# Optimization experiments

Hardware: AMD Instinct MI355X
Metric: run time of the kernel (lower is better)

The kernel has to match this reference:

```python
import jax, jax.numpy as jnp
import numpy as np

DIM_Q = 256
DIM_K = 256
DIM_V = 256
NUM_HEADS = 4


def setup_inputs() -> dict:
    key = jax.random.key(0)
    ks = jax.random.split(key, 12)
    B, NQ, NK = 4, 2048, 2048
    s_in = 1.0 / np.sqrt(DIM_Q)
    s_v = 1.0 / np.sqrt(DIM_V)
    return {
        "Q": jax.random.normal(ks[0], (B, NQ, DIM_Q), jnp.float32),
        "K": jax.random.normal(ks[1], (B, NK, DIM_K), jnp.float32),
        "Wq": jax.random.normal(ks[2], (DIM_V, DIM_Q), jnp.float32) * s_in,
        "bq": jnp.zeros((DIM_V,), jnp.float32),
        "Wk": jax.random.normal(ks[3], (DIM_V, DIM_K), jnp.float32) * s_in,
        "bk": jnp.zeros((DIM_V,), jnp.float32),
        "Wv": jax.random.normal(ks[4], (DIM_V, DIM_K), jnp.float32) * s_in,
        "bv": jnp.zeros((DIM_V,), jnp.float32),
        "Wo": jax.random.normal(ks[5], (DIM_V, DIM_V), jnp.float32) * s_v,
        "bo": jnp.zeros((DIM_V,), jnp.float32),
        "g0": jnp.ones((DIM_V,), jnp.float32),
        "b0": jnp.zeros((DIM_V,), jnp.float32),
        "g1": jnp.ones((DIM_V,), jnp.float32),
        "b1": jnp.zeros((DIM_V,), jnp.float32),
    }


def _layernorm(x, g, b, eps=1e-5):
    mu = jnp.mean(x, axis=-1, keepdims=True)
    var = jnp.mean(jnp.square(x - mu), axis=-1, keepdims=True)
    return (x - mu) * jax.lax.rsqrt(var + eps) * g + b


def _mab(Q, K, Wq, bq, Wk, bk, Wv, bv, Wo, bo, g0, b0, g1, b1):
    B, NQ, _ = Q.shape
    H = NUM_HEADS
    Dh = DIM_V // H  # head dim
    q = jnp.einsum("bqd,ed->bqe", Q, Wq) + bq  # (B,NQ,DV)
    k = jnp.einsum("bkd,ed->bke", K, Wk) + bk
    v = jnp.einsum("bkd,ed->bke", K, Wv) + bv
    # split heads: (B,S,H,Dh) -> (B,H,S,Dh)
    qh = q.reshape(B, NQ, H, Dh).transpose(0, 2, 1, 3)
    kh = k.reshape(B, -1, H, Dh).transpose(0, 2, 1, 3)
    vh = v.reshape(B, -1, H, Dh).transpose(0, 2, 1, 3)
    # NOTE: original scales by sqrt(dim_V), not sqrt(head_dim)
    scores = jnp.einsum("bhqd,bhkd->bhqk", qh, kh) / np.sqrt(DIM_V)
    A = jax.nn.softmax(scores, axis=-1)
    oh = qh + jnp.einsum("bhqk,bhkd->bhqd", A, vh)  # residual with projected Q
    O = oh.transpose(0, 2, 1, 3).reshape(B, NQ, DIM_V)
    O = _layernorm(O, g0, b0)
    O = O + jax.nn.relu(jnp.einsum("bqd,ed->bqe", O, Wo) + bo)
    O = _layernorm(O, g1, b1)
    return O


def reference(Q, K, Wq, bq, Wk, bk, Wv, bv, Wo, bo, g0, b0, g1, b1):
    return _mab(Q, K, Wq, bq, Wk, bk, Wv, bv, Wo, bo, g0, b0, g1, b1)
```

## Files before the change

### kernel.cpp

```cpp
#include <hip/hip_runtime.h>
#include <hip/hip_bf16.h>
#include <math.h>


typedef __attribute__((ext_vector_type(8))) short bf16x8;
typedef __attribute__((ext_vector_type(4))) float f32x4;

static __device__ __forceinline__ unsigned short f2bf(float x) {
  return __bfloat16_as_ushort(__float2bfloat16(x));
}
static __device__ __forceinline__ int pk2(float lo, float hi) {
  return (int)((unsigned)f2bf(lo) | ((unsigned)f2bf(hi) << 16));
}
static __device__ __forceinline__ float exp2_fast(float x) {
  float r; asm("v_exp_f32 %0, %1" : "=v"(r) : "v"(x)); return r;
}

#define SWZ(row, col) ((col) ^ (((row) & 7) << 3))

__global__ __launch_bounds__(256, 2) void proj_kernel(
    const float* __restrict__ Q, const float* __restrict__ K,
    const float* __restrict__ Wq, const float* __restrict__ bq,
    const float* __restrict__ Wk, const float* __restrict__ bk,
    const float* __restrict__ Wv, const float* __restrict__ bv,
    float* __restrict__ qout, unsigned short* __restrict__ kbf,
    unsigned short* __restrict__ vtb)
{
  __shared__ __align__(16) unsigned short Ab[64][64];
  __shared__ __align__(16) unsigned short Wb[64][64];
  const int tid = threadIdx.x;
  const int z = blockIdx.z;
  const int bn = blockIdx.x, bm = blockIdx.y;

  const float* A    = (z == 0) ? Q  : K;
  const float* W    = (z == 0) ? Wq : ((z == 1) ? Wk : Wv);
  const float* bias = (z == 0) ? bq : ((z == 1) ? bk : bv);

  const int wid = tid >> 6, lane = tid & 63;
  const int l15 = lane & 15, g = lane >> 4;
  const int wr = wid >> 1, wc = wid & 1;
  const float* Ablk = A + (size_t)bm * 64 * 256;
  const float* Wblk = W + (size_t)bn * 64 * 256;

  const int sr = tid >> 2, sc = (tid & 3) * 16;
  const int c0 = SWZ(sr, sc), c1 = SWZ(sr, sc + 8);

  f32x4 acc[2][2];
  #pragma unroll
  for (int i = 0; i < 2; ++i)
    #pragma unroll
    for (int j = 0; j < 2; ++j)
      #pragma unroll
      for (int r = 0; r < 4; ++r) acc[i][j][r] = 0.f;

  float4 aR[4], wR[4];
  #pragma unroll
  for (int u = 0; u < 4; ++u) {
    aR[u] = *(const float4*)(Ablk + (size_t)sr*256 + sc + u*4);
    wR[u] = *(const float4*)(Wblk + (size_t)sr*256 + sc + u*4);
  }

  for (int k0 = 0; k0 < 256; k0 += 64) {
    if (k0) __syncthreads();
    int4 pa0 = { pk2(aR[0].x,aR[0].y), pk2(aR[0].z,aR[0].w),
                 pk2(aR[1].x,aR[1].y), pk2(aR[1].z,aR[1].w) };
    int4 pa1 = { pk2(aR[2].x,aR[2].y), pk2(aR[2].z,aR[2].w),
                 pk2(aR[3].x,aR[3].y), pk2(aR[3].z,aR[3].w) };
    int4 pw0 = { pk2(wR[0].x,wR[0].y), pk2(wR[0].z,wR[0].w),
                 pk2(wR[1].x,wR[1].y), pk2(wR[1].z,wR[1].w) };
    int4 pw1 = { pk2(wR[2].x,wR[2].y), pk2(wR[2].z,wR[2].w),
                 pk2(wR[3].x,wR[3].y), pk2(wR[3].z,wR[3].w) };
    *(int4*)&Ab[sr][c0] = pa0;  *(int4*)&Ab[sr][c1] = pa1;
    *(int4*)&Wb[sr][c0] = pw0;  *(int4*)&Wb[sr][c1] = pw1;
    __syncthreads();
    if (k0 < 192) {
      #pragma unroll
      for (int u = 0; u < 4; ++u) {
        aR[u] = *(const float4*)(Ablk + (size_t)sr*256 + (k0+64) + sc + u*4);
        wR[u] = *(const float4*)(Wblk + (size_t)sr*256 + (k0+64) + sc + u*4);
      }
    }
    const unsigned short (*Ta)[64] = (z == 2) ? Wb : Ab;
    const unsigned short (*Tb)[64] = (z == 2) ? Ab : Wb;
    __builtin_amdgcn_s_setprio(1);
    #pragma unroll
    for (int kc = 0; kc < 64; kc += 32) {
      bf16x8 af[2], bf_[2];
      #pragma unroll
      for (int i = 0; i < 2; ++i) {
        int ra = wr*32 + i*16 + l15;
        int rb = wc*32 + i*16 + l15;
        af[i]  = *(const bf16x8*)&Ta[ra][SWZ(ra, kc + g*8)];
        bf_[i] = *(const bf16x8*)&Tb[rb][SWZ(rb, kc + g*8)];
      }
      #pragma unroll
      for (int i = 0; i < 2; ++i)
        #pragma unroll
        for (int j = 0; j < 2; ++j)
          acc[i][j] = __builtin_amdgcn_mfma_f32_16x16x32_bf16(af[i], bf_[j], acc[i][j], 0, 0, 0);
    }
    __builtin_amdgcn_s_setprio(0);
  }

  if (z == 2) {
    const int bvb = bm >> 5;
    const int n0 = (bm & 31) * 64 + wc*32;
    #pragma unroll
    for (int di = 0; di < 2; ++di)
      #pragma unroll
      for (int r = 0; r < 4; ++r) {
        int d = wr*32 + di*16 + g*4 + r;
        float bvs = bias[bn*64 + d];
        #pragma unroll
        for (int ni = 0; ni < 2; ++ni) {
          float c = acc[di][ni][r] + bvs;
          vtb[((size_t)(bvb*4 + bn)*64 + d)*2048 + n0 + ni*16 + l15] = f2bf(c);
        }
      }
    return;
  }

  const int gm = bm*64 + wr*32, ge = bn*64 + wc*32;
  float bv0 = bias[ge + l15], bv1 = bias[ge + 16 + l15];
  #pragma unroll
  for (int mi = 0; mi < 2; ++mi)
    #pragma unroll
    for (int r = 0; r < 4; ++r) {
      int row = gm + mi*16 + g*4 + r;
      #pragma unroll
      for (int ei = 0; ei < 2; ++ei) {
        float c = acc[mi][ei][r] + (ei ? bv1 : bv0);
        if (z == 0) qout[(size_t)row*256 + ge + ei*16 + l15] = c;
        else        kbf [(size_t)row*256 + ge + ei*16 + l15] = f2bf(c);
      }
    }
}

typedef unsigned short tile64_t[64][64];

__global__ __launch_bounds__(512, 4) void attn_mfma6(
    const float* __restrict__ q,
    const unsigned short* __restrict__ kb,
    const unsigned short* __restrict__ vt,
    float* __restrict__ o)
{
  extern __shared__ __align__(16) char smem_dyn[];
  tile64_t* Ks = (tile64_t*)smem_dyn;
  tile64_t* Vt = (tile64_t*)(smem_dyn + 32768);

  const int tid = threadIdx.x;
  const int wid = tid >> 6;
  const int grp = wid >> 2;
  const int w4  = wid & 3;
  const int lane = tid & 63;
  const int l15 = lane & 15;
  const int g = lane >> 4;
  const int lin = blockIdx.x;
  const int xcd = lin & 7, idx = lin >> 3;
  const int bh = xcd * 2 + (idx >> 5);
  const int qb = idx & 31;
  const int b = bh >> 2, h = bh & 3;

  const float qscale = 0.0625f * 1.44269504089f;
  bf16x8 qf[2];
  {
    const float* qp = q + ((size_t)(b*2048 + qb*64 + w4*16 + l15))*256 + h*64;
    #pragma unroll
    for (int ds_ = 0; ds_ < 2; ++ds_) {
      union { bf16x8 v; unsigned short s[8]; } tmp;
      #pragma unroll
      for (int j = 0; j < 8; ++j) tmp.s[j] = f2bf(qp[ds_*32 + g*8 + j] * qscale);
      qf[ds_] = tmp.v;
    }
  }

  const int gt = tid & 255;
  const int sr = gt >> 2, sc = (gt & 3) * 16;
  const int c0 = SWZ(sr, sc), c1 = SWZ(sr, sc + 8);
  const unsigned short* kgp = kb + ((size_t)(b*2048 + grp*1024 + sr))*256 + h*64 + sc;
  const unsigned short* vgp = vt + ((size_t)bh*64 + sr)*2048 + grp*1024 + sc;

  f32x4 oa[4];
  #pragma unroll
  for (int mt = 0; mt < 4; ++mt)
    #pragma unroll
    for (int r = 0; r < 4; ++r) oa[mt][r] = 0.f;
  float l_ = 0.f;

  {
    int4 k0_ = *(const int4*)kgp, k1_ = *(const int4*)(kgp + 8);
    int4 v0_ = *(const int4*)vgp, v1_ = *(const int4*)(vgp + 8);
    *(int4*)&Ks[grp*2+0][sr][c0] = k0_;  *(int4*)&Ks[grp*2+0][sr][c1] = k1_;
    *(int4*)&Vt[grp*2+0][sr][c0] = v0_;  *(int4*)&Vt[grp*2+0][sr][c1] = v1_;
  }
  int4 kA0 = *(const int4*)(kgp + (size_t)64*256);
  int4 kA1 = *(const int4*)(kgp + (size_t)64*256 + 8);
  int4 vA0 = *(const int4*)(vgp + 64);
  int4 vA1 = *(const int4*)(vgp + 64 + 8);
  __syncthreads();

  for (int kt = 0; kt < 16; ++kt) {
    const int cur = kt & 1;
    const tile64_t& Kc = Ks[grp*2 + cur];
    const tile64_t& Vc = Vt[grp*2 + cur];

    f32x4 sa[4];
    #pragma unroll
    for (int mt = 0; mt < 4; ++mt)
      #pragma unroll
      for (int r = 0; r < 4; ++r) sa[mt][r] = 0.f;
    __builtin_amdgcn_s_setprio(1);
    #pragma unroll
    for (int ds_ = 0; ds_ < 2; ++ds_) {
      #pragma unroll
      for (int mt = 0; mt < 4; ++mt) {
        bf16x8 af = *(const bf16x8*)&Kc[mt*16 + l15][SWZ(l15, ds_*32 + g*8)];
        sa[mt] = __builtin_amdgcn_mfma_f32_16x16x32_bf16(af, qf[ds_], sa[mt], 0, 0, 0);
      }
    }
    __builtin_amdgcn_s_setprio(0);

    float ps = 0.f;
    unsigned pk01[4], pk23[4];
    #pragma unroll
    for (int mt = 0; mt < 4; ++mt) {
      float p0 = exp2_fast(sa[mt][0]);
      float p1 = exp2_fast(sa[mt][1]);
      float p2 = exp2_fast(sa[mt][2]);
      float p3 = exp2_fast(sa[mt][3]);
      ps += (p0 + p1) + (p2 + p3);
      pk01[mt] = (unsigned)pk2(p0, p1);
      pk23[mt] = (unsigned)pk2(p2, p3);
    }
    ps += __shfl_xor(ps, 16, 64);
    ps += __shfl_xor(ps, 32, 64);
    l_ += ps;

    __builtin_amdgcn_s_setprio(1);
    #pragma unroll
    for (int ks_ = 0; ks_ < 2; ++ks_) {
      unsigned a0 = pk01[2*ks_], b0 = pk01[2*ks_ + 1];
      unsigned a1 = pk23[2*ks_], b1 = pk23[2*ks_ + 1];
      asm volatile("v_permlane32_swap_b32 %0, %1" : "+v"(a0), "+v"(b0));
      asm volatile("v_permlane16_swap_b32 %0, %1" : "+v"(a0), "+v"(b0));
      asm volatile("v_permlane32_swap_b32 %0, %1" : "+v"(a1), "+v"(b1));
      asm volatile("v_permlane16_swap_b32 %0, %1" : "+v"(a1), "+v"(b1));
      int4 pw = { (int)a0, (int)a1, (int)b0, (int)b1 };
      bf16x8 pf = __builtin_bit_cast(bf16x8, pw);
      #pragma unroll
      for (int mt = 0; mt < 4; ++mt) {
        bf16x8 vf = *(const bf16x8*)&Vc[mt*16 + l15][SWZ(l15, ks_*32 + g*8)];
        oa[mt] = __builtin_amdgcn_mfma_f32_16x16x32_bf16(vf, pf, oa[mt], 0, 0, 0);
      }
    }
    __builtin_amdgcn_s_setprio(0);

    if (kt < 15) {
      *(int4*)&Ks[grp*2+(cur^1)][sr][c0] = kA0;
      *(int4*)&Ks[grp*2+(cur^1)][sr][c1] = kA1;
      *(int4*)&Vt[grp*2+(cur^1)][sr][c0] = vA0;
      *(int4*)&Vt[grp*2+(cur^1)][sr][c1] = vA1;
      if (kt < 14) {
        const unsigned short* kn = kgp + (size_t)(kt + 2) * 64 * 256;
        const unsigned short* vn = vgp + (kt + 2) * 64;
        kA0 = *(const int4*)kn;  kA1 = *(const int4*)(kn + 8);
        vA0 = *(const int4*)vn;  vA1 = *(const int4*)(vn + 8);
      }
    }
    __syncthreads();
  }

  float* cob = (float*)smem_dyn;
  float* cml = (float*)(smem_dyn + 32768);
  const int ci = w4*64 + lane;
  if (grp == 1) {
    #pragma unroll
    for (int mt = 0; mt < 4; ++mt)
      #pragma unroll
      for (int r = 0; r < 4; ++r) cob[(mt*4 + r)*256 + ci] = oa[mt][r];
    cml[ci] = l_;
  }
  __syncthreads();
  if (grp == 0) {
    float linv = 1.0f / (l_ + cml[ci]);
    float* op = o + ((size_t)(b*2048 + qb*64 + w4*16 + l15))*256 + h*64;
    #pragma unroll
    for (int mt = 0; mt < 4; ++mt) {
      int dbase = mt*16 + g*4;
      float4 qv = *(const float4*)(op + dbase);
      float4 st;
      st.x = qv.x + (oa[mt][0] + cob[(mt*4+0)*256 + ci]) * linv;
      st.y = qv.y + (oa[mt][1] + cob[(mt*4+1)*256 + ci]) * linv;
      st.z = qv.z + (oa[mt][2] + cob[(mt*4+2)*256 + ci]) * linv;
      st.w = qv.w + (oa[mt][3] + cob[(mt*4+3)*256 + ci]) * linv;
      *(float4*)(op + dbase) = st;
    }
  }
}

__global__ __launch_bounds__(512) void fused_out(
    const float* __restrict__ x, const float* __restrict__ Wo,
    const float* __restrict__ bo,
    const float* __restrict__ g0v, const float* __restrict__ b0v,
    const float* __restrict__ g1v, const float* __restrict__ b1v,
    float* __restrict__ y)
{
  __shared__ __align__(16) unsigned short As[32][256];
  __shared__ __align__(16) unsigned short Ws[256][64];
  __shared__ float mu_[32], rs_[32];
  float* P = (float*)&Ws[0][0];

  const int tid = threadIdx.x;
  const int w = tid >> 6, lane = tid & 63;
  const int l15 = lane & 15, g = lane >> 4;
  const int r0 = blockIdx.x * 32;

  {
    float4 g4 = *(const float4*)(g0v + lane*4);
    float4 b4 = *(const float4*)(b0v + lane*4);
    #pragma unroll
    for (int rr = 0; rr < 4; ++rr) {
      int m = w*4 + rr;
      const float* xr = x + (size_t)(r0 + m) * 256;
      float4 v = *(const float4*)(xr + lane*4);
      float s = v.x + v.y + v.z + v.w;
      #pragma unroll
      for (int mk = 1; mk <= 32; mk <<= 1) s += __shfl_xor(s, mk, 64);
      float mu = s * (1.0f/256.0f);
      float dx = v.x-mu, dy = v.y-mu, dz = v.z-mu, dw = v.w-mu;
      float qq = dx*dx + dy*dy + dz*dz + dw*dw;
      #pragma unroll
      for (int mk = 1; mk <= 32; mk <<= 1) qq += __shfl_xor(qq, mk, 64);
      float rstd = rsqrtf(qq * (1.0f/256.0f) + 1e-5f);
      if (lane == 0) { mu_[m] = mu; rs_[m] = rstd; }
      float nx = dx*rstd*g4.x + b4.x;
      float ny = dy*rstd*g4.y + b4.y;
      float nz = dz*rstd*g4.z + b4.z;
      float nw = dw*rstd*g4.w + b4.w;
      int2 pv = { pk2(nx, ny), pk2(nz, nw) };
      int col = lane*4;
      *(int2*)&As[m][SWZ(m, col)] = pv;
    }
  }
  __syncthreads();

  const int m0 = (w >> 2) * 16;
  const int e0 = (w & 3) * 64;
  f32x4 acc4[4];
  #pragma unroll
  for (int j = 0; j < 4; ++j)
    #pragma unroll
    for (int r = 0; r < 4; ++r) acc4[j][r] = 0.f;

  for (int k0 = 0; k0 < 256; k0 += 64) {
    if (k0) __syncthreads();
    {
      const int ch = tid & 7;
      const int er = tid >> 3;
      #pragma unroll
      for (int p = 0; p < 4; ++p) {
        int e = p*64 + er;
        const float* wp = Wo + (size_t)e*256 + k0 + ch*8;
        float4 u0 = *(const float4*)wp;
        float4 u1 = *(const float4*)(wp + 4);
        int4 pk = { pk2(u0.x,u0.y), pk2(u0.z,u0.w), pk2(u1.x,u1.y), pk2(u1.z,u1.w) };
        *(int4*)&Ws[e][SWZ(e, ch*8)] = pk;
      }
    }
    __syncthreads();
    __builtin_amdgcn_s_setprio(1);
    #pragma unroll
    for (int ds_ = 0; ds_ < 2; ++ds_) {
      int ma = m0 + l15;
      bf16x8 af = *(const bf16x8*)&As[ma][SWZ(ma, k0 + ds_*32 + g*8)];
      #pragma unroll
      for (int j = 0; j < 4; ++j) {
        int er = e0 + j*16 + l15;
        bf16x8 bfv = *(const bf16x8*)&Ws[er][SWZ(er, ds_*32 + g*8)];
        acc4[j] = __builtin_amdgcn_mfma_f32_16x16x32_bf16(af, bfv, acc4[j], 0, 0, 0);
      }
    }
    __builtin_amdgcn_s_setprio(0);
  }
  __syncthreads();

  #pragma unroll
  for (int j = 0; j < 4; ++j) {
    int e = e0 + j*16 + l15;
    float bov = bo[e], g0e = g0v[e], b0e = b0v[e];
    #pragma unroll
    for (int r = 0; r < 4; ++r) {
      int m = m0 + g*4 + r;
      float xv = x[(size_t)(r0 + m)*256 + e];
      float resv = (xv - mu_[m]) * rs_[m] * g0e + b0e;
      float val = acc4[j][r] + bov;
      P[m*256 + e] = resv + fmaxf(val, 0.f);
    }
  }
  __syncthreads();

  {
    float4 g4 = *(const float4*)(g1v + lane*4);
    float4 b4 = *(const float4*)(b1v + lane*4);
    #pragma unroll
    for (int rr = 0; rr < 4; ++rr) {
      int m = w*4 + rr;
      float4 v = *(const float4*)&P[m*256 + lane*4];
      float s = v.x + v.y + v.z + v.w;
      #pragma unroll
      for (int mk = 1; mk <= 32; mk <<= 1) s += __shfl_xor(s, mk, 64);
      float mu = s * (1.0f/256.0f);
      float dx = v.x-mu, dy = v.y-mu, dz = v.z-mu, dw = v.w-mu;
      float qq = dx*dx + dy*dy + dz*dz + dw*dw;
      #pragma unroll
      for (int mk = 1; mk <= 32; mk <<= 1) qq += __shfl_xor(qq, mk, 64);
      float rstd = rsqrtf(qq * (1.0f/256.0f) + 1e-5f);
      float4 o;
      o.x = dx*rstd*g4.x + b4.x; o.y = dy*rstd*g4.y + b4.y;
      o.z = dz*rstd*g4.z + b4.z; o.w = dw*rstd*g4.w + b4.w;
      *(float4*)(y + (size_t)(r0 + m)*256 + lane*4) = o;
    }
  }
}

extern "C" void kernel_launch(void* const* d_in, const int* in_sizes, int n_in,
                              void* d_out, int out_size, void* d_ws, size_t ws_size,
                              hipStream_t stream) {
  const float* Q  = (const float*)d_in[0];
  const float* K  = (const float*)d_in[1];
  const float* Wq = (const float*)d_in[2];
  const float* bq = (const float*)d_in[3];
  const float* Wk = (const float*)d_in[4];
  const float* bk = (const float*)d_in[5];
  const float* Wv = (const float*)d_in[6];
  const float* bv = (const float*)d_in[7];
  const float* Wo = (const float*)d_in[8];
  const float* bo = (const float*)d_in[9];
  const float* g0 = (const float*)d_in[10];
  const float* b0 = (const float*)d_in[11];
  const float* g1 = (const float*)d_in[12];
  const float* b1 = (const float*)d_in[13];
  float* out = (float*)d_out;

  const size_t SZ = (size_t)4 * 2048 * 256;
  if (ws_size < 2 * SZ * sizeof(unsigned short)) return;

  unsigned short* kbf = (unsigned short*)d_ws;
  unsigned short* vtb = kbf + SZ;

  const int ATTN_LDS = 65536;
  hipFuncSetAttribute((const void*)attn_mfma6,
                      hipFuncAttributeMaxDynamicSharedMemorySize, ATTN_LDS);

  proj_kernel<<<dim3(4, 128, 3), dim3(256), 0, stream>>>(
      Q, K, Wq, bq, Wk, bk, Wv, bv, out, kbf, vtb);
  attn_mfma6<<<dim3(512), dim3(512), ATTN_LDS, stream>>>(out, kbf, vtb, out);
  fused_out<<<dim3(256), dim3(512), 0, stream>>>(out, Wo, bo, g0, b0, g1, b1, out);
}
```

Baseline: 69.56 us.

## Split attention keys four ways with two query tiles per wave

The attention kernel now divides the 2048 keys among four wave-pair groups of 512 keys each, down from two groups of 1024. Each wave handles two 16-row query tiles, so every K/V fragment read from LDS feeds two MFMAs. The double-buffered LDS ring becomes a single buffer per group, refilled from register prefetch with a barrier at the start of each step. The partial sums from the three extra groups are combined through a padded LDS buffer. This is meant to improve LDS operand reuse and raise the MFMA-to-load ratio, at the cost of more accumulator registers, one extra barrier per iteration, and a larger cross-group reduction.

```diff
diff --git a/kernel.cpp b/kernel.cpp
--- a/kernel.cpp
+++ b/kernel.cpp
@@ -136,22 +136,22 @@
     }
 }
 
-typedef unsigned short tile64_t[64][64];
-
-__global__ __launch_bounds__(512, 4) void attn_mfma6(
+typedef unsigned short tileKV_t[64][64];
+
+__global__ __launch_bounds__(512, 4) void attn_mfma7(
     const float* __restrict__ q,
     const unsigned short* __restrict__ kb,
     const unsigned short* __restrict__ vt,
     float* __restrict__ o)
 {
   extern __shared__ __align__(16) char smem_dyn[];
-  tile64_t* Ks = (tile64_t*)smem_dyn;
-  tile64_t* Vt = (tile64_t*)(smem_dyn + 32768);
+  tileKV_t* Ks = (tileKV_t*)smem_dyn;
+  tileKV_t* Vt = (tileKV_t*)(smem_dyn + 32768);
 
   const int tid = threadIdx.x;
   const int wid = tid >> 6;
-  const int grp = wid >> 2;
-  const int w4  = wid & 3;
+  const int grp = wid >> 1;
+  const int qw  = wid & 1;
   const int lane = tid & 63;
   const int l15 = lane & 15;
   const int g = lane >> 4;
@@ -162,138 +162,166 @@
   const int b = bh >> 2, h = bh & 3;
 
   const float qscale = 0.0625f * 1.44269504089f;
-  bf16x8 qf[2];
-  {
-    const float* qp = q + ((size_t)(b*2048 + qb*64 + w4*16 + l15))*256 + h*64;
+  bf16x8 qf[2][2];
+  #pragma unroll
+  for (int qt = 0; qt < 2; ++qt) {
+    const float* qp = q + ((size_t)(b*2048 + qb*64 + qw*32 + qt*16 + l15))*256 + h*64;
     #pragma unroll
     for (int ds_ = 0; ds_ < 2; ++ds_) {
       union { bf16x8 v; unsigned short s[8]; } tmp;
       #pragma unroll
       for (int j = 0; j < 8; ++j) tmp.s[j] = f2bf(qp[ds_*32 + g*8 + j] * qscale);
-      qf[ds_] = tmp.v;
-    }
-  }
-
-  const int gt = tid & 255;
-  const int sr = gt >> 2, sc = (gt & 3) * 16;
-  const int c0 = SWZ(sr, sc), c1 = SWZ(sr, sc + 8);
-  const unsigned short* kgp = kb + ((size_t)(b*2048 + grp*1024 + sr))*256 + h*64 + sc;
-  const unsigned short* vgp = vt + ((size_t)bh*64 + sr)*2048 + grp*1024 + sc;
-
-  f32x4 oa[4];
-  #pragma unroll
-  for (int mt = 0; mt < 4; ++mt)
-    #pragma unroll
-    for (int r = 0; r < 4; ++r) oa[mt][r] = 0.f;
-  float l_ = 0.f;
-
-  {
-    int4 k0_ = *(const int4*)kgp, k1_ = *(const int4*)(kgp + 8);
-    int4 v0_ = *(const int4*)vgp, v1_ = *(const int4*)(vgp + 8);
-    *(int4*)&Ks[grp*2+0][sr][c0] = k0_;  *(int4*)&Ks[grp*2+0][sr][c1] = k1_;
-    *(int4*)&Vt[grp*2+0][sr][c0] = v0_;  *(int4*)&Vt[grp*2+0][sr][c1] = v1_;
-  }
-  int4 kA0 = *(const int4*)(kgp + (size_t)64*256);
-  int4 kA1 = *(const int4*)(kgp + (size_t)64*256 + 8);
-  int4 vA0 = *(const int4*)(vgp + 64);
-  int4 vA1 = *(const int4*)(vgp + 64 + 8);
+      qf[qt][ds_] = tmp.v;
+    }
+  }
+
+  const int gt = tid & 127;
+  const int srow = gt >> 1;
+  const int chs  = (gt & 1) * 32;
+  int wcol[4];
+  #pragma unroll
+  for (int j = 0; j < 4; ++j) wcol[j] = SWZ(srow, chs + 8*j);
+  const unsigned short* kgp = kb + ((size_t)(b*2048 + grp*512 + srow))*256 + h*64 + chs;
+  const unsigned short* vgp = vt + ((size_t)bh*64 + srow)*2048 + grp*512 + chs;
+
+  f32x4 oa[2][4];
+  #pragma unroll
+  for (int qt = 0; qt < 2; ++qt)
+    #pragma unroll
+    for (int mt = 0; mt < 4; ++mt)
+      #pragma unroll
+      for (int r = 0; r < 4; ++r) oa[qt][mt][r] = 0.f;
+  float l0 = 0.f, l1 = 0.f;
+
+  int4 kR[4], vR[4];
+  #pragma unroll
+  for (int j = 0; j < 4; ++j) {
+    kR[j] = *(const int4*)(kgp + 8*j);
+    vR[j] = *(const int4*)(vgp + 8*j);
+  }
+
+  for (int t = 0; t < 8; ++t) {
+    if (t) __syncthreads();
+    #pragma unroll
+    for (int j = 0; j < 4; ++j) *(int4*)&Ks[grp][srow][wcol[j]] = kR[j];
+    #pragma unroll
+    for (int j = 0; j < 4; ++j) *(int4*)&Vt[grp][srow][wcol[j]] = vR[j];
+    __syncthreads();
+    if (t < 7) {
+      #pragma unroll
+      for (int j = 0; j < 4; ++j)
+        kR[j] = *(const int4*)(kgp + (size_t)(t+1)*64*256 + 8*j);
+    }
+
+    f32x4 sa[2][4];
+    #pragma unroll
+    for (int qt = 0; qt < 2; ++qt)
+      #pragma unroll
+      for (int mt = 0; mt < 4; ++mt)
+        #pragma unroll
+        for (int r = 0; r < 4; ++r) sa[qt][mt][r] = 0.f;
+    __builtin_amdgcn_s_setprio(1);
+    #pragma unroll
+    for (int ds_ = 0; ds_ < 2; ++ds_) {
+      #pragma unroll
+      for (int mt = 0; mt < 4; ++mt) {
+        bf16x8 af = *(const bf16x8*)&Ks[grp][mt*16 + l15][SWZ(l15, ds_*32 + g*8)];
+        sa[0][mt] = __builtin_amdgcn_mfma_f32_16x16x32_bf16(af, qf[0][ds_], sa[0][mt], 0, 0, 0);
+        sa[1][mt] = __builtin_amdgcn_mfma_f32_16x16x32_bf16(af, qf[1][ds_], sa[1][mt], 0, 0, 0);
+      }
+    }
+    __builtin_amdgcn_s_setprio(0);
+
+    unsigned pk01[2][4], pk23[2][4];
+    #pragma unroll
+    for (int qt = 0; qt < 2; ++qt) {
+      float ps = 0.f;
+      #pragma unroll
+      for (int mt = 0; mt < 4; ++mt) {
+        float p0 = exp2_fast(sa[qt][mt][0]);
+        float p1 = exp2_fast(sa[qt][mt][1]);
+        float p2 = exp2_fast(sa[qt][mt][2]);
+        float p3 = exp2_fast(sa[qt][mt][3]);
+        ps += (p0 + p1) + (p2 + p3);
+        pk01[qt][mt] = (unsigned)pk2(p0, p1);
+        pk23[qt][mt] = (unsigned)pk2(p2, p3);
+      }
+      ps += __shfl_xor(ps, 16, 64);
+      ps += __shfl_xor(ps, 32, 64);
+      if (qt == 0) l0 += ps; else l1 += ps;
+    }
+
+    if (t < 7) {
+      #pragma unroll
+      for (int j = 0; j < 4; ++j)
+        vR[j] = *(const int4*)(vgp + (t+1)*64 + 8*j);
+    }
+
+    __builtin_amdgcn_s_setprio(1);
+    #pragma unroll
+    for (int ks_ = 0; ks_ < 2; ++ks_) {
+      bf16x8 pf[2];
+      #pragma unroll
+      for (int qt = 0; qt < 2; ++qt) {
+        unsigned a0 = pk01[qt][2*ks_], b0 = pk01[qt][2*ks_ + 1];
+        unsigned a1 = pk23[qt][2*ks_], b1 = pk23[qt][2*ks_ + 1];
+        asm volatile("v_permlane32_swap_b32 %0, %1" : "+v"(a0), "+v"(b0));
+        asm volatile("v_permlane16_swap_b32 %0, %1" : "+v"(a0), "+v"(b0));
+        asm volatile("v_permlane32_swap_b32 %0, %1" : "+v"(a1), "+v"(b1));
+        asm volatile("v_permlane16_swap_b32 %0, %1" : "+v"(a1), "+v"(b1));
+        int4 pw = { (int)a0, (int)a1, (int)b0, (int)b1 };
+        pf[qt] = __builtin_bit_cast(bf16x8, pw);
+      }
+      #pragma unroll
+      for (int mt = 0; mt < 4; ++mt) {
+        bf16x8 vf = *(const bf16x8*)&Vt[grp][mt*16 + l15][SWZ(l15, ks_*32 + g*8)];
+        oa[0][mt] = __builtin_amdgcn_mfma_f32_16x16x32_bf16(vf, pf[0], oa[0][mt], 0, 0, 0);
+        oa[1][mt] = __builtin_amdgcn_mfma_f32_16x16x32_bf16(vf, pf[1], oa[1][mt], 0, 0, 0);
+      }
+    }
+    __builtin_amdgcn_s_setprio(0);
+  }
+
   __syncthreads();
-
-  for (int kt = 0; kt < 16; ++kt) {
-    const int cur = kt & 1;
-    const tile64_t& Kc = Ks[grp*2 + cur];
-    const tile64_t& Vc = Vt[grp*2 + cur];
-
-    f32x4 sa[4];
-    #pragma unroll
-    for (int mt = 0; mt < 4; ++mt)
-      #pragma unroll
-      for (int r = 0; r < 4; ++r) sa[mt][r] = 0.f;
-    __builtin_amdgcn_s_setprio(1);
-    #pragma unroll
-    for (int ds_ = 0; ds_ < 2; ++ds_) {
-      #pragma unroll
-      for (int mt = 0; mt < 4; ++mt) {
-        bf16x8 af = *(const bf16x8*)&Kc[mt*16 + l15][SWZ(l15, ds_*32 + g*8)];
-        sa[mt] = __builtin_amdgcn_mfma_f32_16x16x32_bf16(af, qf[ds_], sa[mt], 0, 0, 0);
-      }
-    }
-    __builtin_amdgcn_s_setprio(0);
-
-    float ps = 0.f;
-    unsigned pk01[4], pk23[4];
-    #pragma unroll
-    for (int mt = 0; mt < 4; ++mt) {
-      float p0 = exp2_fast(sa[mt][0]);
-      float p1 = exp2_fast(sa[mt][1]);
-      float p2 = exp2_fast(sa[mt][2]);
-      float p3 = exp2_fast(sa[mt][3]);
-      ps += (p0 + p1) + (p2 + p3);
-      pk01[mt] = (unsigned)pk2(p0, p1);
-      pk23[mt] = (unsigned)pk2(p2, p3);
-    }
-    ps += __shfl_xor(ps, 16, 64);
-    ps += __shfl_xor(ps, 32, 64);
-    l_ += ps;
-
-    __builtin_amdgcn_s_setprio(1);
-    #pragma unroll
-    for (int ks_ = 0; ks_ < 2; ++ks_) {
-      unsigned a0 = pk01[2*ks_], b0 = pk01[2*ks_ + 1];
-      unsigned a1 = pk23[2*ks_], b1 = pk23[2*ks_ + 1];
-      asm volatile("v_permlane32_swap_b32 %0, %1" : "+v"(a0), "+v"(b0));
-      asm volatile("v_permlane16_swap_b32 %0, %1" : "+v"(a0), "+v"(b0));
-      asm volatile("v_permlane32_swap_b32 %0, %1" : "+v"(a1), "+v"(b1));
-      asm volatile("v_permlane16_swap_b32 %0, %1" : "+v"(a1), "+v"(b1));
-      int4 pw = { (int)a0, (int)a1, (int)b0, (int)b1 };
-      bf16x8 pf = __builtin_bit_cast(bf16x8, pw);
-      #pragma unroll
-      for (int mt = 0; mt < 4; ++mt) {
-        bf16x8 vf = *(const bf16x8*)&Vc[mt*16 + l15][SWZ(l15, ks_*32 + g*8)];
-        oa[mt] = __builtin_amdgcn_mfma_f32_16x16x32_bf16(vf, pf, oa[mt], 0, 0, 0);
-      }
-    }
-    __builtin_amdgcn_s_setprio(0);
-
-    if (kt < 15) {
-      *(int4*)&Ks[grp*2+(cur^1)][sr][c0] = kA0;
-      *(int4*)&Ks[grp*2+(cur^1)][sr][c1] = kA1;
-      *(int4*)&Vt[grp*2+(cur^1)][sr][c0] = vA0;
-      *(int4*)&Vt[grp*2+(cur^1)][sr][c1] = vA1;
-      if (kt < 14) {
-        const unsigned short* kn = kgp + (size_t)(kt + 2) * 64 * 256;
-        const unsigned short* vn = vgp + (kt + 2) * 64;
-        kA0 = *(const int4*)kn;  kA1 = *(const int4*)(kn + 8);
-        vA0 = *(const int4*)vn;  vA1 = *(const int4*)(vn + 8);
-      }
-    }
-    __syncthreads();
-  }
-
   float* cob = (float*)smem_dyn;
-  float* cml = (float*)(smem_dyn + 32768);
-  const int ci = w4*64 + lane;
-  if (grp == 1) {
-    #pragma unroll
-    for (int mt = 0; mt < 4; ++mt)
-      #pragma unroll
-      for (int r = 0; r < 4; ++r) cob[(mt*4 + r)*256 + ci] = oa[mt][r];
-    cml[ci] = l_;
+  float* cml = (float*)(smem_dyn + 3*64*65*4);
+  if (grp > 0) {
+    const int gi = grp - 1;
+    #pragma unroll
+    for (int qt = 0; qt < 2; ++qt) {
+      int qloc = qw*32 + qt*16 + l15;
+      #pragma unroll
+      for (int mt = 0; mt < 4; ++mt)
+        #pragma unroll
+        for (int r = 0; r < 4; ++r)
+          cob[(gi*64 + mt*16 + g*4 + r)*65 + qloc] = oa[qt][mt][r];
+      cml[gi*64 + qloc] = (qt == 0) ? l0 : l1;
+    }
   }
   __syncthreads();
   if (grp == 0) {
-    float linv = 1.0f / (l_ + cml[ci]);
-    float* op = o + ((size_t)(b*2048 + qb*64 + w4*16 + l15))*256 + h*64;
-    #pragma unroll
-    for (int mt = 0; mt < 4; ++mt) {
-      int dbase = mt*16 + g*4;
-      float4 qv = *(const float4*)(op + dbase);
-      float4 st;
-      st.x = qv.x + (oa[mt][0] + cob[(mt*4+0)*256 + ci]) * linv;
-      st.y = qv.y + (oa[mt][1] + cob[(mt*4+1)*256 + ci]) * linv;
-      st.z = qv.z + (oa[mt][2] + cob[(mt*4+2)*256 + ci]) * linv;
-      st.w = qv.w + (oa[mt][3] + cob[(mt*4+3)*256 + ci]) * linv;
-      *(float4*)(op + dbase) = st;
+    #pragma unroll
+    for (int qt = 0; qt < 2; ++qt) {
+      int qloc = qw*32 + qt*16 + l15;
+      float lsum = (qt == 0 ? l0 : l1)
+                 + cml[qloc] + cml[64 + qloc] + cml[128 + qloc];
+      float linv = 1.0f / lsum;
+      float* op = o + ((size_t)(b*2048 + qb*64 + qloc))*256 + h*64;
+      #pragma unroll
+      for (int mt = 0; mt < 4; ++mt) {
+        int dbase = mt*16 + g*4;
+        float4 qv = *(const float4*)(op + dbase);
+        float4 st;
+        #pragma unroll
+        for (int r = 0; r < 4; ++r) {
+          float s = oa[qt][mt][r]
+                  + cob[(0*64 + dbase + r)*65 + qloc]
+                  + cob[(1*64 + dbase + r)*65 + qloc]
+                  + cob[(2*64 + dbase + r)*65 + qloc];
+          ((float*)&st)[r] = ((const float*)&qv)[r] + s * linv;
+        }
+        *(float4*)(op + dbase) = st;
+      }
     }
   }
 }
@@ -449,11 +477,11 @@
   unsigned short* vtb = kbf + SZ;
 
   const int ATTN_LDS = 65536;
-  hipFuncSetAttribute((const void*)attn_mfma6,
+  hipFuncSetAttribute((const void*)attn_mfma7,
                       hipFuncAttributeMaxDynamicSharedMemorySize, ATTN_LDS);
 
   proj_kernel<<<dim3(4, 128, 3), dim3(256), 0, stream>>>(
       Q, K, Wq, bq, Wk, bk, Wv, bv, out, kbf, vtb);
-  attn_mfma6<<<dim3(512), dim3(512), ATTN_LDS, stream>>>(out, kbf, vtb, out);
+  attn_mfma7<<<dim3(512), dim3(512), ATTN_LDS, stream>>>(out, kbf, vtb, out);
   fused_out<<<dim3(256), dim3(512), 0, stream>>>(out, Wo, bo, g0, b0, g1, b1, out);
 }
```

New measurement: 125.8 us. +80.9%, slower.

## Keep full-K input row block resident in LDS and reuse across two output tiles

Applied to the files above, without the earlier changes.

The projection kernel now converts and stores the whole 64x256 input row block to LDS once, then loops over two output column tiles per block, halving the grid in x. This cuts redundant global reads and bf16 conversion of Q/K rows, which were previously repeated for each of four column tiles. In exchange the software prefetch of the next K-chunk into registers is removed, so weight loads are no longer overlapped with MFMA. LDS use per block also rises, and there are fewer blocks.

```diff
diff --git a/kernel.cpp b/kernel.cpp
--- a/kernel.cpp
+++ b/kernel.cpp
@@ -18,7 +18,9 @@
 
 #define SWZ(row, col) ((col) ^ (((row) & 7) << 3))
 
-__global__ __launch_bounds__(256, 2) void proj_kernel(
+typedef unsigned short tile64_t[64][64];
+
+__global__ __launch_bounds__(256, 2) void proj2_kernel(
     const float* __restrict__ Q, const float* __restrict__ K,
     const float* __restrict__ Wq, const float* __restrict__ bq,
     const float* __restrict__ Wk, const float* __restrict__ bk,
@@ -26,11 +28,11 @@
     float* __restrict__ qout, unsigned short* __restrict__ kbf,
     unsigned short* __restrict__ vtb)
 {
-  __shared__ __align__(16) unsigned short Ab[64][64];
+  __shared__ __align__(16) unsigned short Ab[64][256];
   __shared__ __align__(16) unsigned short Wb[64][64];
   const int tid = threadIdx.x;
   const int z = blockIdx.z;
-  const int bn = blockIdx.x, bm = blockIdx.y;
+  const int bm = blockIdx.y;
 
   const float* A    = (z == 0) ? Q  : K;
   const float* W    = (z == 0) ? Wq : ((z == 1) ? Wk : Wv);
@@ -40,103 +42,104 @@
   const int l15 = lane & 15, g = lane >> 4;
   const int wr = wid >> 1, wc = wid & 1;
   const float* Ablk = A + (size_t)bm * 64 * 256;
-  const float* Wblk = W + (size_t)bn * 64 * 256;
 
   const int sr = tid >> 2, sc = (tid & 3) * 16;
   const int c0 = SWZ(sr, sc), c1 = SWZ(sr, sc + 8);
 
-  f32x4 acc[2][2];
   #pragma unroll
-  for (int i = 0; i < 2; ++i)
-    #pragma unroll
-    for (int j = 0; j < 2; ++j)
-      #pragma unroll
-      for (int r = 0; r < 4; ++r) acc[i][j][r] = 0.f;
-
-  float4 aR[4], wR[4];
-  #pragma unroll
-  for (int u = 0; u < 4; ++u) {
-    aR[u] = *(const float4*)(Ablk + (size_t)sr*256 + sc + u*4);
-    wR[u] = *(const float4*)(Wblk + (size_t)sr*256 + sc + u*4);
-  }
-
-  for (int k0 = 0; k0 < 256; k0 += 64) {
-    if (k0) __syncthreads();
-    int4 pa0 = { pk2(aR[0].x,aR[0].y), pk2(aR[0].z,aR[0].w),
-                 pk2(aR[1].x,aR[1].y), pk2(aR[1].z,aR[1].w) };
-    int4 pa1 = { pk2(aR[2].x,aR[2].y), pk2(aR[2].z,aR[2].w),
-                 pk2(aR[3].x,aR[3].y), pk2(aR[3].z,aR[3].w) };
-    int4 pw0 = { pk2(wR[0].x,wR[0].y), pk2(wR[0].z,wR[0].w),
-                 pk2(wR[1].x,wR[1].y), pk2(wR[1].z,wR[1].w) };
-    int4 pw1 = { pk2(wR[2].x,wR[2].y), pk2(wR[2].z,wR[2].w),
-                 pk2(wR[3].x,wR[3].y), pk2(wR[3].z,wR[3].w) };
-    *(int4*)&Ab[sr][c0] = pa0;  *(int4*)&Ab[sr][c1] = pa1;
-    *(int4*)&Wb[sr][c0] = pw0;  *(int4*)&Wb[sr][c1] = pw1;
-    __syncthreads();
-    if (k0 < 192) {
-      #pragma unroll
-      for (int u = 0; u < 4; ++u) {
-        aR[u] = *(const float4*)(Ablk + (size_t)sr*256 + (k0+64) + sc + u*4);
-        wR[u] = *(const float4*)(Wblk + (size_t)sr*256 + (k0+64) + sc + u*4);
-      }
-    }
-    const unsigned short (*Ta)[64] = (z == 2) ? Wb : Ab;
-    const unsigned short (*Tb)[64] = (z == 2) ? Ab : Wb;
-    __builtin_amdgcn_s_setprio(1);
-    #pragma unroll
-    for (int kc = 0; kc < 64; kc += 32) {
-      bf16x8 af[2], bf_[2];
-      #pragma unroll
-      for (int i = 0; i < 2; ++i) {
-        int ra = wr*32 + i*16 + l15;
-        int rb = wc*32 + i*16 + l15;
-        af[i]  = *(const bf16x8*)&Ta[ra][SWZ(ra, kc + g*8)];
-        bf_[i] = *(const bf16x8*)&Tb[rb][SWZ(rb, kc + g*8)];
-      }
-      #pragma unroll
-      for (int i = 0; i < 2; ++i)
+  for (int kb = 0; kb < 4; ++kb) {
+    const float* ap = Ablk + (size_t)sr*256 + kb*64 + sc;
+    float4 a0 = *(const float4*)ap,       a1 = *(const float4*)(ap + 4);
+    float4 a2 = *(const float4*)(ap + 8), a3 = *(const float4*)(ap + 12);
+    int4 p0 = { pk2(a0.x,a0.y), pk2(a0.z,a0.w), pk2(a1.x,a1.y), pk2(a1.z,a1.w) };
+    int4 p1 = { pk2(a2.x,a2.y), pk2(a2.z,a2.w), pk2(a3.x,a3.y), pk2(a3.z,a3.w) };
+    *(int4*)&Ab[sr][kb*64 + c0] = p0;
+    *(int4*)&Ab[sr][kb*64 + c1] = p1;
+  }
+
+  for (int bi = 0; bi < 2; ++bi) {
+    const int bn = blockIdx.x + bi*2;
+    const float* Wblk = W + (size_t)bn * 64 * 256;
+
+    f32x4 acc[2][2];
+    #pragma unroll
+    for (int i = 0; i < 2; ++i)
+      #pragma unroll
+      for (int j = 0; j < 2; ++j)
         #pragma unroll
-        for (int j = 0; j < 2; ++j)
-          acc[i][j] = __builtin_amdgcn_mfma_f32_16x16x32_bf16(af[i], bf_[j], acc[i][j], 0, 0, 0);
-    }
-    __builtin_amdgcn_s_setprio(0);
-  }
-
-  if (z == 2) {
-    const int bvb = bm >> 5;
-    const int n0 = (bm & 31) * 64 + wc*32;
-    #pragma unroll
-    for (int di = 0; di < 2; ++di)
-      #pragma unroll
-      for (int r = 0; r < 4; ++r) {
-        int d = wr*32 + di*16 + g*4 + r;
-        float bvs = bias[bn*64 + d];
+        for (int r = 0; r < 4; ++r) acc[i][j][r] = 0.f;
+
+    for (int k0 = 0; k0 < 256; k0 += 64) {
+      if (bi | k0) __syncthreads();
+      {
+        const float* wp = Wblk + (size_t)sr*256 + k0 + sc;
+        float4 w0 = *(const float4*)wp,       w1 = *(const float4*)(wp + 4);
+        float4 w2 = *(const float4*)(wp + 8), w3 = *(const float4*)(wp + 12);
+        int4 p0 = { pk2(w0.x,w0.y), pk2(w0.z,w0.w), pk2(w1.x,w1.y), pk2(w1.z,w1.w) };
+        int4 p1 = { pk2(w2.x,w2.y), pk2(w2.z,w2.w), pk2(w3.x,w3.y), pk2(w3.z,w3.w) };
+        *(int4*)&Wb[sr][c0] = p0;
+        *(int4*)&Wb[sr][c1] = p1;
+      }
+      __syncthreads();
+
+      __builtin_amdgcn_s_setprio(1);
+      #pragma unroll
+      for (int kc = 0; kc < 64; kc += 32) {
+        bf16x8 af[2], bf_[2];
         #pragma unroll
-        for (int ni = 0; ni < 2; ++ni) {
-          float c = acc[di][ni][r] + bvs;
-          vtb[((size_t)(bvb*4 + bn)*64 + d)*2048 + n0 + ni*16 + l15] = f2bf(c);
+        for (int i = 0; i < 2; ++i) {
+          int ra = wr*32 + i*16 + l15;
+          int rb = wc*32 + i*16 + l15;
+          if (z == 2) {
+            af[i]  = *(const bf16x8*)&Wb[ra][SWZ(ra, kc + g*8)];
+            bf_[i] = *(const bf16x8*)&Ab[rb][k0 + SWZ(rb, kc + g*8)];
+          } else {
+            af[i]  = *(const bf16x8*)&Ab[ra][k0 + SWZ(ra, kc + g*8)];
+            bf_[i] = *(const bf16x8*)&Wb[rb][SWZ(rb, kc + g*8)];
+          }
         }
-      }
-    return;
-  }
-
-  const int gm = bm*64 + wr*32, ge = bn*64 + wc*32;
-  float bv0 = bias[ge + l15], bv1 = bias[ge + 16 + l15];
-  #pragma unroll
-  for (int mi = 0; mi < 2; ++mi)
-    #pragma unroll
-    for (int r = 0; r < 4; ++r) {
-      int row = gm + mi*16 + g*4 + r;
-      #pragma unroll
-      for (int ei = 0; ei < 2; ++ei) {
-        float c = acc[mi][ei][r] + (ei ? bv1 : bv0);
-        if (z == 0) qout[(size_t)row*256 + ge + ei*16 + l15] = c;
-        else        kbf [(size_t)row*256 + ge + ei*16 + l15] = f2bf(c);
-      }
-    }
-}
-
-typedef unsigned short tile64_t[64][64];
+        #pragma unroll
+        for (int i = 0; i < 2; ++i)
+          #pragma unroll
+          for (int j = 0; j < 2; ++j)
+            acc[i][j] = __builtin_amdgcn_mfma_f32_16x16x32_bf16(af[i], bf_[j], acc[i][j], 0, 0, 0);
+      }
+      __builtin_amdgcn_s_setprio(0);
+    }
+
+    if (z == 2) {
+      const int bvb = bm >> 5;
+      const int n0 = (bm & 31) * 64 + wc*32;
+      #pragma unroll
+      for (int di = 0; di < 2; ++di)
+        #pragma unroll
+        for (int r = 0; r < 4; ++r) {
+          int d = wr*32 + di*16 + g*4 + r;
+          float bvs = bias[bn*64 + d];
+          #pragma unroll
+          for (int ni = 0; ni < 2; ++ni) {
+            float c = acc[di][ni][r] + bvs;
+            vtb[((size_t)(bvb*4 + bn)*64 + d)*2048 + n0 + ni*16 + l15] = f2bf(c);
+          }
+        }
+    } else {
+      const int gm = bm*64 + wr*32, ge = bn*64 + wc*32;
+      float bv0 = bias[ge + l15], bv1 = bias[ge + 16 + l15];
+      #pragma unroll
+      for (int mi = 0; mi < 2; ++mi)
+        #pragma unroll
+        for (int r = 0; r < 4; ++r) {
+          int row = gm + mi*16 + g*4 + r;
+          #pragma unroll
+          for (int ei = 0; ei < 2; ++ei) {
+            float c = acc[mi][ei][r] + (ei ? bv1 : bv0);
+            if (z == 0) qout[(size_t)row*256 + ge + ei*16 + l15] = c;
+            else        kbf [(size_t)row*256 + ge + ei*16 + l15] = f2bf(c);
+          }
+        }
+    }
+  }
+}
 
 __global__ __launch_bounds__(512, 4) void attn_mfma6(
     const float* __restrict__ q,
@@ -338,8 +341,7 @@
       float nz = dz*rstd*g4.z + b4.z;
       float nw = dw*rstd*g4.w + b4.w;
       int2 pv = { pk2(nx, ny), pk2(nz, nw) };
-      int col = lane*4;
-      *(int2*)&As[m][SWZ(m, col)] = pv;
+      *(int2*)&As[m][SWZ(m, lane*4)] = pv;
     }
   }
   __syncthreads();
@@ -452,7 +454,7 @@
   hipFuncSetAttribute((const void*)attn_mfma6,
                       hipFuncAttributeMaxDynamicSharedMemorySize, ATTN_LDS);
 
-  proj_kernel<<<dim3(4, 128, 3), dim3(256), 0, stream>>>(
+  proj2_kernel<<<dim3(2, 128, 3), dim3(256), 0, stream>>>(
       Q, K, Wq, bq, Wk, bk, Wv, bv, out, kbf, vtb);
   attn_mfma6<<<dim3(512), dim3(512), ATTN_LDS, stream>>>(out, kbf, vtb, out);
   fused_out<<<dim3(256), dim3(512), 0, stream>>>(out, Wo, bo, g0, b0, g1, b1, out);
```

New measurement: 68.01 us. 2.2% less time.
